# Optimization experiments

Hardware: AMD Instinct MI355X
Metric: run time of the kernel (lower is better)

The kernel has to match this reference:

```python
import jax, jax.numpy as jnp
import numpy as np

H = 96  # hidden size


def setup_inputs() -> dict:
    key = jax.random.key(0)
    ks = jax.random.split(key, 7)
    T, B = 16384, 32
    s = 1.0 / np.sqrt(H)
    return {
        "x": jax.random.normal(ks[0], (T, B, 1), dtype=jnp.float32),
        "w_ih": jax.random.normal(ks[1], (4 * H, 1), dtype=jnp.float32) * s,
        "w_hh": jax.random.normal(ks[2], (4 * H, H), dtype=jnp.float32) * s,
        "b_ih": jax.random.normal(ks[3], (4 * H,), dtype=jnp.float32) * s,
        "b_hh": jax.random.normal(ks[4], (4 * H,), dtype=jnp.float32) * s,
        "fc_w": jax.random.normal(ks[5], (1, H), dtype=jnp.float32) * s,
        "fc_b": jax.random.normal(ks[6], (1,), dtype=jnp.float32) * s,
    }


def reference(x, w_ih, w_hh, b_ih, b_hh, fc_w, fc_b):
    # x: [T, B, 1] (time-major, like nn.LSTM with batch_first=False)
    T, B, _ = x.shape
    res = x[:, :, 0:1]
    # Precompute the input contribution to the gates for all timesteps: [T, B, 4H]
    gates_x = jnp.einsum('tbi,gi->tbg', x, w_ih) + b_ih + b_hh

    def step(carry, gx):
        h, c = carry  # [B, H] each
        g = gx + h @ w_hh.T  # [B, 4H]
        i, f, gg, o = jnp.split(g, 4, axis=-1)  # PyTorch gate order i|f|g|o
        i = jax.nn.sigmoid(i)
        f = jax.nn.sigmoid(f)
        gg = jnp.tanh(gg)
        o = jax.nn.sigmoid(o)
        c = f * c + i * gg
        h = o * jnp.tanh(c)
        return (h, c), h

    h0 = jnp.zeros((B, H), dtype=x.dtype)  # hidden=None -> zero init
    c0 = jnp.zeros((B, H), dtype=x.dtype)
    _, hs = jax.lax.scan(step, (h0, c0), gates_x)  # hs: [T, B, H]
    # FullyConnected(x) + residual
    return jnp.einsum('tbh,oh->tbo', hs, fc_w) + fc_b + res
```

## Files before the change

kernel.cpp:

```cpp
#include <hip/hip_runtime.h>


constexpr int HH   = 96;
constexpr int BB   = 32;
constexpr int TT   = 16384;
constexpr int TH   = 512;
constexpr int NS   = 512;
constexpr int ROWP = 104;

typedef _Float16 f16x8 __attribute__((ext_vector_type(8)));
typedef _Float16 f16x2 __attribute__((ext_vector_type(2)));
typedef float    f32x4 __attribute__((ext_vector_type(4)));

template <int CTRL>
__device__ __forceinline__ float dpp_bcast(float v) {
    int r = __builtin_amdgcn_mov_dpp(__builtin_bit_cast(int, v), CTRL, 0xF, 0xF, true);
    return __builtin_bit_cast(float, r);
}
constexpr int DPP_B1 = 0x55;
constexpr int DPP_B2 = 0xAA;
constexpr int DPP_B3 = 0xFF;

#define LOG2E 1.44269504f

__attribute__((amdgpu_flat_work_group_size(TH, TH)))
__global__ void lstm_kernel(const float* __restrict__ x,
                            const float* __restrict__ w_ih,
                            const float* __restrict__ w_hh,
                            const float* __restrict__ b_ih,
                            const float* __restrict__ b_hh,
                            const float* __restrict__ fc_w,
                            const float* __restrict__ fc_b,
                            float* __restrict__ out) {
    __shared__ __align__(16) _Float16 hist[(NS + 1) * ROWP];
    __shared__ __align__(16) float xs[NS];
    __shared__ float fcw_s[HH];

    const int tid = threadIdx.x;
    const int b   = blockIdx.x;
    const int wv  = tid >> 6;
    const int l   = tid & 63;
    const int h16 = l >> 4;
    const int rIn = l & 15;
    const int s   = rIn & 3;
    const int q   = rIn >> 2;
    const int te  = (h16 == 3) ? 2 : h16;
    const int j   = 12 * wv + 4 * te + q;

    const float ek_s = (s == 2) ? (-2.0f * LOG2E) : (-LOG2E);
    f16x8 Bw[3][3];
#pragma unroll
    for (int t = 0; t < 3; ++t) {
        const float* wrow = w_hh + (s * HH + 12 * wv + 4 * t + q) * HH;
#pragma unroll
        for (int kt = 0; kt < 3; ++kt) {
            const float* wr = wrow + kt * 32 + 8 * h16;
            f16x8 v;
#pragma unroll
            for (int e = 0; e < 8; ++e) v[e] = (_Float16)(wr[e] * ek_s);
            Bw[t][kt] = v;
        }
    }
#pragma unroll
    for (int t = 0; t < 3; ++t)
#pragma unroll
        for (int kt = 0; kt < 3; ++kt) asm volatile("" : "+v"(Bw[t][kt]));

    const float wih2  = w_ih[s * HH + j] * ek_s;
    const float bias2 = (b_ih[s * HH + j] + b_hh[s * HH + j]) * ek_s;
    const float a_mul = (s == 2) ? (-4.0f * LOG2E) : 1.0f;
    const float a_add = (s == 2) ? (2.0f * LOG2E) : 0.0f;
    const bool  te1 = (h16 == 1), te2 = (h16 >= 2);

    const float fcb = fc_b[0];
    float c = 0.0f;

    for (int i = tid; i < HH; i += TH) fcw_s[i] = fc_w[i];

    auto flush = [&](int t0) {
        for (int i = tid; i < NS; i += TH) {
            const uint2* hr = (const uint2*)(hist + (i + 1) * ROWP);
            float a = 0.0f;
#pragma unroll
            for (int m = 0; m < 24; ++m) {
                uint2 u = hr[m];
                f16x2 p0 = __builtin_bit_cast(f16x2, u.x);
                f16x2 p1 = __builtin_bit_cast(f16x2, u.y);
                a = fmaf((float)p0.x, fcw_s[4 * m + 0], a);
                a = fmaf((float)p0.y, fcw_s[4 * m + 1], a);
                a = fmaf((float)p1.x, fcw_s[4 * m + 2], a);
                a = fmaf((float)p1.y, fcw_s[4 * m + 3], a);
            }
            out[(t0 + i) * BB + b] = a + fcb + xs[i];
        }
    };

    const _Float16* rd_p;
    _Float16*       wr_p;

    auto step = [&](float gx, const int ofs) {
        const uint4* p = (const uint4*)(rd_p + ofs);
        uint4 u0 = p[0], u1 = p[4], u2 = p[8];
        const f16x8 a0 = __builtin_bit_cast(f16x8, u0);
        const f16x8 a1 = __builtin_bit_cast(f16x8, u1);
        const f16x8 a2 = __builtin_bit_cast(f16x8, u2);

        const f32x4 cz = {gx, 0.f, 0.f, 0.f};
        f32x4 acc[3] = {cz, cz, cz};
#pragma unroll
        for (int t = 0; t < 3; ++t)
            acc[t] = __builtin_amdgcn_mfma_f32_16x16x32_f16(a0, Bw[t][0], acc[t], 0, 0, 0);
#pragma unroll
        for (int t = 0; t < 3; ++t)
            acc[t] = __builtin_amdgcn_mfma_f32_16x16x32_f16(a1, Bw[t][1], acc[t], 0, 0, 0);
#pragma unroll
        for (int t = 0; t < 3; ++t)
            acc[t] = __builtin_amdgcn_mfma_f32_16x16x32_f16(a2, Bw[t][2], acc[t], 0, 0, 0);

        float pre = te1 ? acc[1][0] : acc[0][0];
        pre       = te2 ? acc[2][0] : pre;

        const float act =
            fmaf(__builtin_amdgcn_rcpf(1.0f + __builtin_amdgcn_exp2f(pre)),
                 a_mul, a_add);
        const float fv = dpp_bcast<DPP_B1>(act);
        const float gv = dpp_bcast<DPP_B2>(act);
        const float ov = dpp_bcast<DPP_B3>(act);
        c = fmaf(fv, c, act * gv);
        const float rt = __builtin_amdgcn_rcpf(1.0f + __builtin_amdgcn_exp2f(c));
        const float h  = fmaf(ov + ov, rt, -ov);
        if (s == 0 && h16 < 3) *(wr_p + ofs) = (_Float16)h;
        __syncthreads();
    };

    for (int w = 0; w < TT / NS; ++w) {
        const int t0 = w * NS;
        if (w == 0) {
            if (tid < 48) ((uint32_t*)hist)[tid] = 0u;
        } else {
            flush(t0 - NS);
            if (tid < 48)
                ((uint32_t*)hist)[tid] = ((const uint32_t*)(hist + NS * ROWP))[tid];
        }
        __syncthreads();
        for (int i = tid; i < NS; i += TH) xs[i] = x[(t0 + i) * BB + b];
        __syncthreads();

        rd_p = hist + 8 * h16;
        wr_p = hist + ROWP + j;
        for (int tt = 0; tt < NS; tt += 4) {
            const float4 xq = *(const float4*)(xs + tt);
            const float gx0 = fmaf(xq.x, wih2, bias2);
            const float gx1 = fmaf(xq.y, wih2, bias2);
            const float gx2 = fmaf(xq.z, wih2, bias2);
            const float gx3 = fmaf(xq.w, wih2, bias2);
            step(gx0, 0 * ROWP);
            step(gx1, 1 * ROWP);
            step(gx2, 2 * ROWP);
            step(gx3, 3 * ROWP);
            rd_p += 4 * ROWP;
            wr_p += 4 * ROWP;
        }
    }
    flush(TT - NS);
}

extern "C" void kernel_launch(void* const* d_in, const int* in_sizes, int n_in,
                              void* d_out, int out_size, void* d_ws, size_t ws_size,
                              hipStream_t stream) {
    const float* x    = (const float*)d_in[0];
    const float* w_ih = (const float*)d_in[1];
    const float* w_hh = (const float*)d_in[2];
    const float* b_ih = (const float*)d_in[3];
    const float* b_hh = (const float*)d_in[4];
    const float* fc_w = (const float*)d_in[5];
    const float* fc_b = (const float*)d_in[6];
    float* out = (float*)d_out;

    lstm_kernel<<<dim3(BB), dim3(TH), 0, stream>>>(x, w_ih, w_hh, b_ih, b_hh,
                                                   fc_w, fc_b, out);
}
```

Before: 4.581 ms.

## Spread hidden units over 12 waves with two MFMA tiles each, unroll by 8

After: 4.968 ms. 1.08x slower.

```diff
diff --git a/kernel.cpp b/kernel.cpp
--- a/kernel.cpp
+++ b/kernel.cpp
@@ -4,7 +4,7 @@
 constexpr int HH   = 96;
 constexpr int BB   = 32;
 constexpr int TT   = 16384;
-constexpr int TH   = 512;
+constexpr int TH   = 768;
 constexpr int NS   = 512;
 constexpr int ROWP = 104;
 
@@ -44,14 +44,14 @@
     const int rIn = l & 15;
     const int s   = rIn & 3;
     const int q   = rIn >> 2;
-    const int te  = (h16 == 3) ? 2 : h16;
-    const int j   = 12 * wv + 4 * te + q;
+    const int te  = h16 & 1;
+    const int j   = 8 * wv + 4 * te + q;
 
     const float ek_s = (s == 2) ? (-2.0f * LOG2E) : (-LOG2E);
-    f16x8 Bw[3][3];
+    f16x8 Bw[2][3];
 #pragma unroll
-    for (int t = 0; t < 3; ++t) {
-        const float* wrow = w_hh + (s * HH + 12 * wv + 4 * t + q) * HH;
+    for (int t = 0; t < 2; ++t) {
+        const float* wrow = w_hh + (s * HH + 8 * wv + 4 * t + q) * HH;
 #pragma unroll
         for (int kt = 0; kt < 3; ++kt) {
             const float* wr = wrow + kt * 32 + 8 * h16;
@@ -62,7 +62,7 @@
         }
     }
 #pragma unroll
-    for (int t = 0; t < 3; ++t)
+    for (int t = 0; t < 2; ++t)
 #pragma unroll
         for (int kt = 0; kt < 3; ++kt) asm volatile("" : "+v"(Bw[t][kt]));
 
@@ -70,7 +70,7 @@
     const float bias2 = (b_ih[s * HH + j] + b_hh[s * HH + j]) * ek_s;
     const float a_mul = (s == 2) ? (-4.0f * LOG2E) : 1.0f;
     const float a_add = (s == 2) ? (2.0f * LOG2E) : 0.0f;
-    const bool  te1 = (h16 == 1), te2 = (h16 >= 2);
+    const bool  te1 = (te == 1);
 
     const float fcb = fc_b[0];
     float c = 0.0f;
@@ -106,19 +106,18 @@
         const f16x8 a2 = __builtin_bit_cast(f16x8, u2);
 
         const f32x4 cz = {gx, 0.f, 0.f, 0.f};
-        f32x4 acc[3] = {cz, cz, cz};
+        f32x4 acc[2] = {cz, cz};
 #pragma unroll
-        for (int t = 0; t < 3; ++t)
+        for (int t = 0; t < 2; ++t)
             acc[t] = __builtin_amdgcn_mfma_f32_16x16x32_f16(a0, Bw[t][0], acc[t], 0, 0, 0);
 #pragma unroll
-        for (int t = 0; t < 3; ++t)
+        for (int t = 0; t < 2; ++t)
             acc[t] = __builtin_amdgcn_mfma_f32_16x16x32_f16(a1, Bw[t][1], acc[t], 0, 0, 0);
 #pragma unroll
-        for (int t = 0; t < 3; ++t)
+        for (int t = 0; t < 2; ++t)
             acc[t] = __builtin_amdgcn_mfma_f32_16x16x32_f16(a2, Bw[t][2], acc[t], 0, 0, 0);
 
-        float pre = te1 ? acc[1][0] : acc[0][0];
-        pre       = te2 ? acc[2][0] : pre;
+        const float pre = te1 ? acc[1][0] : acc[0][0];
 
         const float act =
             fmaf(__builtin_amdgcn_rcpf(1.0f + __builtin_amdgcn_exp2f(pre)),
@@ -129,7 +128,7 @@
         c = fmaf(fv, c, act * gv);
         const float rt = __builtin_amdgcn_rcpf(1.0f + __builtin_amdgcn_exp2f(c));
         const float h  = fmaf(ov + ov, rt, -ov);
-        if (s == 0 && h16 < 3) *(wr_p + ofs) = (_Float16)h;
+        if (s == 0 && h16 < 2) *(wr_p + ofs) = (_Float16)h;
         __syncthreads();
     };
 
@@ -148,18 +147,27 @@
 
         rd_p = hist + 8 * h16;
         wr_p = hist + ROWP + j;
-        for (int tt = 0; tt < NS; tt += 4) {
-            const float4 xq = *(const float4*)(xs + tt);
-            const float gx0 = fmaf(xq.x, wih2, bias2);
-            const float gx1 = fmaf(xq.y, wih2, bias2);
-            const float gx2 = fmaf(xq.z, wih2, bias2);
-            const float gx3 = fmaf(xq.w, wih2, bias2);
-            step(gx0, 0 * ROWP);
-            step(gx1, 1 * ROWP);
-            step(gx2, 2 * ROWP);
-            step(gx3, 3 * ROWP);
-            rd_p += 4 * ROWP;
-            wr_p += 4 * ROWP;
+        for (int tt = 0; tt < NS; tt += 8) {
+            const float4 xq0 = *(const float4*)(xs + tt);
+            const float4 xq1 = *(const float4*)(xs + tt + 4);
+            const float g0 = fmaf(xq0.x, wih2, bias2);
+            const float g1 = fmaf(xq0.y, wih2, bias2);
+            const float g2 = fmaf(xq0.z, wih2, bias2);
+            const float g3 = fmaf(xq0.w, wih2, bias2);
+            const float g4 = fmaf(xq1.x, wih2, bias2);
+            const float g5 = fmaf(xq1.y, wih2, bias2);
+            const float g6 = fmaf(xq1.z, wih2, bias2);
+            const float g7 = fmaf(xq1.w, wih2, bias2);
+            step(g0, 0 * ROWP);
+            step(g1, 1 * ROWP);
+            step(g2, 2 * ROWP);
+            step(g3, 3 * ROWP);
+            step(g4, 4 * ROWP);
+            step(g5, 5 * ROWP);
+            step(g6, 6 * ROWP);
+            step(g7, 7 * ROWP);
+            rd_p += 8 * ROWP;
+            wr_p += 8 * ROWP;
         }
     }
     flush(TT - NS);
```
